# Optimization experiments

Measured on AMD Instinct MI355X. Metric: run time of the kernel, lower is better.

## Reference

```python
import jax, jax.numpy as jnp
import numpy as np

B, T, D = 2, 4096, 2048
H, DH = 4, 32


def setup_inputs() -> dict:
    key = jax.random.key(0)
    k0, k1, k2, k3 = jax.random.split(key, 4)
    return {
        "hidden_states": jax.random.normal(k0, (B, T, D), dtype=jnp.float32),
        "Wq": jax.random.normal(k1, (H * DH, D), dtype=jnp.float32) * 0.02,
        "Ww": jax.random.normal(k2, (H, D), dtype=jnp.float32) * 0.02,
        "Wk": jax.random.normal(k3, (DH, D), dtype=jnp.float32) * 0.02,
    }


def reference(hidden_states, Wq, Ww, Wk):
    b, t, d = hidden_states.shape
    h, dh = Ww.shape[0], Wk.shape[0]
    # projections (nn.Linear: x @ W^T)
    q = (hidden_states @ Wq.T).reshape(b, t, h, dh)  # (B,T,H,Dh)
    w = hidden_states @ Ww.T                          # (B,T,H)
    k = hidden_states @ Wk.T                          # (B,T,Dh) shared across heads
    # multi-head QK^T -> ReLU -> per-head weighted sum (no softmax)
    raw = jnp.einsum('bthd,bsd->bths', q, k)          # (B,T,H,S)
    raw = jax.nn.relu(raw)
    index_scores = jnp.einsum('bths,bth->bts', raw, w)  # (B,T,S)
    return index_scores
```

## Files before the change

kernel.cpp:

```cpp
#include <hip/hip_runtime.h>
#include <hip/hip_bf16.h>

#define B_ 2
#define T_ 4096
#define D_ 2048
#define H_ 4
#define NC 176
#define ROWS (B_ * T_)
#define TILE_E (16 * NC)
#define WTILE_E (16 * D_)

typedef __attribute__((ext_vector_type(8))) short short8;
typedef __attribute__((ext_vector_type(4))) short short4v;
typedef __attribute__((ext_vector_type(4))) float f32x4;
typedef __attribute__((ext_vector_type(4))) float float4v;

__device__ inline unsigned short f2bf(float f) {
  unsigned u = __float_as_uint(f);
  u += 0x7fffu + ((u >> 16) & 1u);
  return (unsigned short)(u >> 16);
}
__device__ inline float bf2f(unsigned short s) {
  return __uint_as_float(((unsigned)s) << 16);
}

__global__ __launch_bounds__(256) void pack_weights(const float* __restrict__ Wq,
                                                    const float* __restrict__ Ww,
                                                    const float* __restrict__ Wk,
                                                    unsigned short* __restrict__ Wcb) {
  int row = blockIdx.x;
  int cg  = threadIdx.x;
  int col = cg * 8;

  const float* src = nullptr;
  if (row < 128)       src = Wq + (size_t)row * D_;
  else if (row < 160)  src = Wk + (size_t)(row - 128) * D_;
  else if (row < 164)  src = Ww + (size_t)(row - 160) * D_;

  short8 v;
  if (src) {
    float4v f0 = *(const float4v*)(src + col);
    float4v f1 = *(const float4v*)(src + col + 4);
#pragma unroll
    for (int i = 0; i < 4; ++i) {
      v[i]     = (short)f2bf(f0[i]);
      v[i + 4] = (short)f2bf(f1[i]);
    }
  } else {
#pragma unroll
    for (int i = 0; i < 8; ++i) v[i] = 0;
  }
  int n = row >> 4, r = row & 15;
  *(short8*)&Wcb[(size_t)n * WTILE_E + (size_t)cg * 128 + r * 8] = v;
}

__global__ __launch_bounds__(512, 2) void proj_kernel(const float* __restrict__ hs,
                                                      const unsigned short* __restrict__ Wcb,
                                                      unsigned short* __restrict__ Cb) {
  __shared__ f32x4 red[8][11][64];

  int wid  = threadIdx.x >> 6;
  int lane = threadIdx.x & 63;
  int lr = lane & 15, lo = lane >> 4;
  int row0 = blockIdx.x * 32;
  int k0   = wid * 256;

  const float* ap0 = hs + (size_t)(row0 + lr) * D_ + k0 + lo * 8;
  const float* ap1 = ap0 + (size_t)16 * D_;
  const unsigned short* bbase = Wcb + (size_t)k0 * 16 + lo * 128 + lr * 8;

  f32x4 acc0[11], acc1[11];
#pragma unroll
  for (int n = 0; n < 11; ++n) {
    acc0[n] = (f32x4){0.f, 0.f, 0.f, 0.f};
    acc1[n] = (f32x4){0.f, 0.f, 0.f, 0.f};
  }

  float4v Am0[2][2], Am1[2][2];
  short8  Bv[2][11];

  Am0[0][0] = *(const float4v*)(ap0);
  Am0[0][1] = *(const float4v*)(ap0 + 4);
  Am1[0][0] = *(const float4v*)(ap1);
  Am1[0][1] = *(const float4v*)(ap1 + 4);
#pragma unroll
  for (int n = 0; n < 11; ++n)
    Bv[0][n] = *(const short8*)(bbase + (size_t)n * WTILE_E);

#pragma unroll
  for (int s = 0; s < 8; ++s) {
    const int cur = s & 1, nxt = cur ^ 1;
    if (s < 7) {
      Am0[nxt][0] = *(const float4v*)(ap0 + (s + 1) * 32);
      Am0[nxt][1] = *(const float4v*)(ap0 + (s + 1) * 32 + 4);
      Am1[nxt][0] = *(const float4v*)(ap1 + (s + 1) * 32);
      Am1[nxt][1] = *(const float4v*)(ap1 + (s + 1) * 32 + 4);
#pragma unroll
      for (int n = 0; n < 11; ++n)
        Bv[nxt][n] = *(const short8*)(bbase + (size_t)n * WTILE_E + (s + 1) * 512);
    }
    short8 a0, a1;
#pragma unroll
    for (int i = 0; i < 4; ++i) {
      a0[i]     = (short)f2bf(Am0[cur][0][i]);
      a0[i + 4] = (short)f2bf(Am0[cur][1][i]);
      a1[i]     = (short)f2bf(Am1[cur][0][i]);
      a1[i + 4] = (short)f2bf(Am1[cur][1][i]);
    }
#pragma unroll
    for (int n = 0; n < 11; ++n) {
      acc0[n] = __builtin_amdgcn_mfma_f32_16x16x32_bf16(a0, Bv[cur][n], acc0[n], 0, 0, 0);
      acc1[n] = __builtin_amdgcn_mfma_f32_16x16x32_bf16(a1, Bv[cur][n], acc1[n], 0, 0, 0);
    }
  }

#pragma unroll
  for (int ph = 0; ph < 2; ++ph) {
#pragma unroll
    for (int n = 0; n < 11; ++n)
      red[wid][n][lane] = ph == 0 ? acc0[n] : acc1[n];
    __syncthreads();
    unsigned short* cb = Cb + (size_t)((row0 >> 4) + ph) * TILE_E + (lr & 7);
#pragma unroll
    for (int g = 0; g < 2; ++g) {
      int n = wid + g * 8;
      if (n < 11) {
        f32x4 t = red[0][n][lane];
#pragma unroll
        for (int w = 1; w < 8; ++w) {
          f32x4 p = red[w][n][lane];
#pragma unroll
          for (int r = 0; r < 4; ++r) t[r] += p[r];
        }
        int oct = n * 2 + (lr >> 3);
#pragma unroll
        for (int r = 0; r < 4; ++r)
          cb[oct * 128 + (lo * 4 + r) * 8] = f2bf(t[r]);
      }
    }
    __syncthreads();
  }
}

__global__ __launch_bounds__(256) void score_kernel(const unsigned short* __restrict__ Cb,
                                                    float* __restrict__ out) {
  int b = blockIdx.z, tb = blockIdx.y, sb = blockIdx.x;
  int wid  = threadIdx.x >> 6;
  int lane = threadIdx.x & 63;
  int lr = lane & 15, lo = lane >> 4;
  int wm = wid >> 1, wn = wid & 1;
  int t_base = tb * 128 + wm * 64;
  int s_base = sb * 128 + wn * 64;

  const unsigned short* C2 = Cb + (size_t)b * (T_ / 16) * TILE_E;
  float* O = out + (size_t)b * T_ * T_;

  short8 bf[4];
#pragma unroll
  for (int n = 0; n < 4; ++n)
    bf[n] = *(const short8*)(C2 + (size_t)((s_base >> 4) + n) * TILE_E +
                             (16 + lo) * 128 + lr * 8);

  const f32x4 zero = (f32x4){0.f, 0.f, 0.f, 0.f};

  short8  af[2][H_];
  short4v w4v[2];

  {
    const unsigned short* Ct0 = C2 + (size_t)(t_base >> 4) * TILE_E;
#pragma unroll
    for (int h = 0; h < H_; ++h)
      af[0][h] = *(const short8*)(Ct0 + (h * 4 + lo) * 128 + lr * 8);
    w4v[0] = *(const short4v*)(Ct0 + 20 * 128 + lo * 32);
  }

#pragma unroll
  for (int m = 0; m < 4; ++m) {
    const int cur = m & 1, nxt = cur ^ 1;
    if (m < 3) {
      const unsigned short* Ctn = C2 + (size_t)((t_base >> 4) + m + 1) * TILE_E;
#pragma unroll
      for (int h = 0; h < H_; ++h)
        af[nxt][h] = *(const short8*)(Ctn + (h * 4 + lo) * 128 + lr * 8);
      w4v[nxt] = *(const short4v*)(Ctn + 20 * 128 + lo * 32);
    }

    const unsigned short* Ct = C2 + (size_t)((t_base >> 4) + m) * TILE_E;
    float wv[4][H_];
    {
      short4v w0 = w4v[cur];
#pragma unroll
      for (int h = 0; h < H_; ++h) wv[0][h] = bf2f((unsigned short)w0[h]);
#pragma unroll
      for (int r = 1; r < 4; ++r) {
        short4v wr = *(const short4v*)(Ct + 20 * 128 + lo * 32 + r * 8);
#pragma unroll
        for (int h = 0; h < H_; ++h) wv[r][h] = bf2f((unsigned short)wr[h]);
      }
    }

    int tc = t_base + m * 16 + lo * 4;
    float* rowp[4];
#pragma unroll
    for (int r = 0; r < 4; ++r)
      rowp[r] = O + (size_t)(tc + r) * T_ + s_base + lr;

#pragma unroll
    for (int n = 0; n < 4; ++n) {
      f32x4 o = zero;
#pragma unroll
      for (int h = 0; h < H_; ++h) {
        f32x4 c = __builtin_amdgcn_mfma_f32_16x16x32_bf16(af[cur][h], bf[n], zero, 0, 0, 0);
#pragma unroll
        for (int r = 0; r < 4; ++r) o[r] += wv[r][h] * fmaxf(c[r], 0.f);
      }
#pragma unroll
      for (int r = 0; r < 4; ++r)
        rowp[r][n * 16] = o[r];
    }
  }
}

extern "C" void kernel_launch(void* const* d_in, const int* in_sizes, int n_in,
                              void* d_out, int out_size, void* d_ws, size_t ws_size,
                              hipStream_t stream) {
  const float* hs = (const float*)d_in[0];
  const float* Wq = (const float*)d_in[1];
  const float* Ww = (const float*)d_in[2];
  const float* Wk = (const float*)d_in[3];
  float* out = (float*)d_out;

  unsigned short* Wcb = (unsigned short*)d_ws;
  unsigned short* Cb  = (unsigned short*)((char*)d_ws + (1 << 20));

  pack_weights<<<NC, 256, 0, stream>>>(Wq, Ww, Wk, Wcb);
  proj_kernel<<<ROWS / 32, 512, 0, stream>>>(hs, Wcb, Cb);
  dim3 g(T_ / 128, T_ / 128, B_);
  score_kernel<<<g, 256, 0, stream>>>(Cb, out);
}
```

Baseline: 60.09 us.

## Retile score kernel to 16-row by 512-column blocks with one t-tile per block

The score kernel now gives each block a single 16-row t tile and 512 s columns, with each wave covering 128 columns, replacing the 128x128 block made of 64x64 wave tiles. The t-loop and the double-buffering of the q/w fragments go away. Each wave now loads 8 k fragments and only one set of q fragments and weights. Each block writes 16 full 512-float row segments, which may improve write locality for the output store that dominates the kernel. The cost is less reuse of the k fragments across t rows and a larger grid.

```diff
diff --git a/kernel.cpp b/kernel.cpp
--- a/kernel.cpp
+++ b/kernel.cpp
@@ -144,80 +144,57 @@
 
 __global__ __launch_bounds__(256) void score_kernel(const unsigned short* __restrict__ Cb,
                                                     float* __restrict__ out) {
-  int b = blockIdx.z, tb = blockIdx.y, sb = blockIdx.x;
+  int b = blockIdx.z;
   int wid  = threadIdx.x >> 6;
   int lane = threadIdx.x & 63;
   int lr = lane & 15, lo = lane >> 4;
-  int wm = wid >> 1, wn = wid & 1;
-  int t_base = tb * 128 + wm * 64;
-  int s_base = sb * 128 + wn * 64;
+  int t_base = blockIdx.y * 16;
+  int s_base = blockIdx.x * 512 + wid * 128;
 
   const unsigned short* C2 = Cb + (size_t)b * (T_ / 16) * TILE_E;
   float* O = out + (size_t)b * T_ * T_;
 
-  short8 bf[4];
-#pragma unroll
-  for (int n = 0; n < 4; ++n)
+  const unsigned short* Ct = C2 + (size_t)(t_base >> 4) * TILE_E;
+
+  short8 af[H_];
+#pragma unroll
+  for (int h = 0; h < H_; ++h)
+    af[h] = *(const short8*)(Ct + (h * 4 + lo) * 128 + lr * 8);
+
+  float wv[4][H_];
+#pragma unroll
+  for (int r = 0; r < 4; ++r) {
+    short4v wr = *(const short4v*)(Ct + 20 * 128 + lo * 32 + r * 8);
+#pragma unroll
+    for (int h = 0; h < H_; ++h) wv[r][h] = bf2f((unsigned short)wr[h]);
+  }
+
+  short8 bf[8];
+#pragma unroll
+  for (int n = 0; n < 8; ++n)
     bf[n] = *(const short8*)(C2 + (size_t)((s_base >> 4) + n) * TILE_E +
                              (16 + lo) * 128 + lr * 8);
 
   const f32x4 zero = (f32x4){0.f, 0.f, 0.f, 0.f};
 
-  short8  af[2][H_];
-  short4v w4v[2];
-
-  {
-    const unsigned short* Ct0 = C2 + (size_t)(t_base >> 4) * TILE_E;
-#pragma unroll
-    for (int h = 0; h < H_; ++h)
-      af[0][h] = *(const short8*)(Ct0 + (h * 4 + lo) * 128 + lr * 8);
-    w4v[0] = *(const short4v*)(Ct0 + 20 * 128 + lo * 32);
-  }
-
-#pragma unroll
-  for (int m = 0; m < 4; ++m) {
-    const int cur = m & 1, nxt = cur ^ 1;
-    if (m < 3) {
-      const unsigned short* Ctn = C2 + (size_t)((t_base >> 4) + m + 1) * TILE_E;
-#pragma unroll
-      for (int h = 0; h < H_; ++h)
-        af[nxt][h] = *(const short8*)(Ctn + (h * 4 + lo) * 128 + lr * 8);
-      w4v[nxt] = *(const short4v*)(Ctn + 20 * 128 + lo * 32);
-    }
-
-    const unsigned short* Ct = C2 + (size_t)((t_base >> 4) + m) * TILE_E;
-    float wv[4][H_];
-    {
-      short4v w0 = w4v[cur];
-#pragma unroll
-      for (int h = 0; h < H_; ++h) wv[0][h] = bf2f((unsigned short)w0[h]);
-#pragma unroll
-      for (int r = 1; r < 4; ++r) {
-        short4v wr = *(const short4v*)(Ct + 20 * 128 + lo * 32 + r * 8);
-#pragma unroll
-        for (int h = 0; h < H_; ++h) wv[r][h] = bf2f((unsigned short)wr[h]);
-      }
-    }
-
-    int tc = t_base + m * 16 + lo * 4;
-    float* rowp[4];
+  int tc = t_base + lo * 4;
+  float* rowp[4];
+#pragma unroll
+  for (int r = 0; r < 4; ++r)
+    rowp[r] = O + (size_t)(tc + r) * T_ + s_base + lr;
+
+#pragma unroll
+  for (int n = 0; n < 8; ++n) {
+    f32x4 o = zero;
+#pragma unroll
+    for (int h = 0; h < H_; ++h) {
+      f32x4 c = __builtin_amdgcn_mfma_f32_16x16x32_bf16(af[h], bf[n], zero, 0, 0, 0);
+#pragma unroll
+      for (int r = 0; r < 4; ++r) o[r] += wv[r][h] * fmaxf(c[r], 0.f);
+    }
 #pragma unroll
     for (int r = 0; r < 4; ++r)
-      rowp[r] = O + (size_t)(tc + r) * T_ + s_base + lr;
-
-#pragma unroll
-    for (int n = 0; n < 4; ++n) {
-      f32x4 o = zero;
-#pragma unroll
-      for (int h = 0; h < H_; ++h) {
-        f32x4 c = __builtin_amdgcn_mfma_f32_16x16x32_bf16(af[cur][h], bf[n], zero, 0, 0, 0);
-#pragma unroll
-        for (int r = 0; r < 4; ++r) o[r] += wv[r][h] * fmaxf(c[r], 0.f);
-      }
-#pragma unroll
-      for (int r = 0; r < 4; ++r)
-        rowp[r][n * 16] = o[r];
-    }
+      rowp[r][n * 16] = o[r];
   }
 }
 
@@ -235,6 +212,6 @@
 
   pack_weights<<<NC, 256, 0, stream>>>(Wq, Ww, Wk, Wcb);
   proj_kernel<<<ROWS / 32, 512, 0, stream>>>(hs, Wcb, Cb);
-  dim3 g(T_ / 128, T_ / 128, B_);
+  dim3 g(T_ / 512, T_ / 16, B_);
   score_kernel<<<g, 256, 0, stream>>>(Cb, out);
 }
```

After: 56.57 us. 5.8% less time.
